# Kernel optimization log

Hardware: AMD Instinct MI355X
Metric: run time of the kernel (lower is better)

Reference implementation:

```python
import jax, jax.numpy as jnp
import numpy as np

N, E = 50000, 800000
F_IN, HID, H, LBL = 512, 16, 8, 40
HC = HID * H  # 128
BN_EPS = 1e-5
ELU_ALPHA = 0.2
NEG_SLOPE = 0.2


def setup_inputs() -> dict:
    key = jax.random.key(0)
    ks = jax.random.split(key, 32)
    inp = {}
    inp['x'] = jax.random.normal(ks[0], (N, F_IN), dtype=jnp.float32)
    inp['edge_index'] = jax.random.randint(ks[1], (2, E), 0, N, dtype=jnp.int32)
    # layer 0: F_IN -> (H, HID), concat
    inp['W0'] = jax.random.normal(ks[2], (F_IN, HC), dtype=jnp.float32) * 0.05
    inp['as0'] = jax.random.normal(ks[3], (H, HID), dtype=jnp.float32) * 0.1
    inp['ad0'] = jax.random.normal(ks[4], (H, HID), dtype=jnp.float32) * 0.1
    inp['b0'] = jnp.zeros((HC,), jnp.float32)
    inp['g0'] = jnp.ones((HC,), jnp.float32)
    inp['be0'] = jnp.zeros((HC,), jnp.float32)
    inp['rm0'] = jnp.zeros((HC,), jnp.float32)
    inp['rv0'] = jnp.ones((HC,), jnp.float32)
    # layer 1: HC -> (H, HID), concat
    inp['W1'] = jax.random.normal(ks[5], (HC, HC), dtype=jnp.float32) * 0.1
    inp['as1'] = jax.random.normal(ks[6], (H, HID), dtype=jnp.float32) * 0.1
    inp['ad1'] = jax.random.normal(ks[7], (H, HID), dtype=jnp.float32) * 0.1
    inp['b1'] = jnp.zeros((HC,), jnp.float32)
    inp['g1'] = jnp.ones((HC,), jnp.float32)
    inp['be1'] = jnp.zeros((HC,), jnp.float32)
    inp['rm1'] = jnp.zeros((HC,), jnp.float32)
    inp['rv1'] = jnp.ones((HC,), jnp.float32)
    # layer 2: HC -> (1, LBL), mean (concat=False)
    inp['W2'] = jax.random.normal(ks[8], (HC, LBL), dtype=jnp.float32) * 0.1
    inp['as2'] = jax.random.normal(ks[9], (1, LBL), dtype=jnp.float32) * 0.1
    inp['ad2'] = jax.random.normal(ks[10], (1, LBL), dtype=jnp.float32) * 0.1
    inp['b2'] = jnp.zeros((LBL,), jnp.float32)
    return inp


def _gat_conv(xf, src, dst, W, a_src, a_dst, b, heads, out_ch, concat):
    # PyG GATConv (eval): linear -> per-head attn logits -> segment softmax over dst -> scatter-add
    n = xf.shape[0]
    h = (xf @ W).reshape(n, heads, out_ch)            # [N,H,C]
    alpha_s = jnp.einsum('nhc,hc->nh', h, a_src)      # [N,H]
    alpha_d = jnp.einsum('nhc,hc->nh', h, a_dst)
    e = jax.nn.leaky_relu(alpha_s[src] + alpha_d[dst], NEG_SLOPE)  # [Etot,H]
    m = jax.ops.segment_max(e, dst, num_segments=n)
    e = jnp.exp(e - m[dst])
    s = jax.ops.segment_sum(e, dst, num_segments=n)
    alpha = e / (s[dst] + 1e-16)                      # [Etot,H]
    msg = alpha[:, :, None] * h[src]                  # [Etot,H,C]
    out = jax.ops.segment_sum(msg, dst, num_segments=n)  # [N,H,C]
    out = out.reshape(n, heads * out_ch) if concat else out.mean(axis=1)
    return out + b


def _bn_elu(xf, g, be, rm, rv):
    y = (xf - rm) * (g * jax.lax.rsqrt(rv + BN_EPS)) + be
    return jnp.where(y > 0, y, ELU_ALPHA * jnp.expm1(y))


def reference(x, edge_index, W0, as0, ad0, b0, g0, be0, rm0, rv0,
              W1, as1, ad1, b1, g1, be1, rm1, rv1, W2, as2, ad2, b2):
    n = x.shape[0]
    # add self-loops (PyG GATConv default add_self_loops=True)
    loops = jnp.arange(n, dtype=edge_index.dtype)
    src = jnp.concatenate([edge_index[0], loops])
    dst = jnp.concatenate([edge_index[1], loops])
    h = _gat_conv(x, src, dst, W0, as0, ad0, b0, H, HID, True)
    h = _bn_elu(h, g0, be0, rm0, rv0)
    h = _gat_conv(h, src, dst, W1, as1, ad1, b1, H, HID, True)
    h = _bn_elu(h, g1, be1, rm1, rv1)
    out = _gat_conv(h, src, dst, W2, as2, ad2, b2, 1, LBL, False)
    return out
```

## Files before the change

kernel.cpp:

```cpp
#include <hip/hip_runtime.h>
#include <hip/hip_bf16.h>
#include <cstdint>
#include <cstddef>

#define NN 50000
#define EE 800000
#define FIN 512
#define HIDC 16
#define NH 8
#define HCH 128
#define NLBL 40
#define NLBLP 48
#define ETOT (EE + NN)
#define NEG_SLOPE 0.2f
#define ELU_A 0.2f
#define BN_EPS 1e-5f
#define SCH 8192
#define NCHK 7

typedef __attribute__((ext_vector_type(8))) short bf16x8;
typedef __attribute__((ext_vector_type(4))) short bf16x4;
typedef __attribute__((ext_vector_type(4))) float f32x4;

__device__ inline short f2b(float f) {
    __hip_bfloat16 h = __float2bfloat16(f);
    return *reinterpret_cast<short*>(&h);
}
__device__ inline float blo(unsigned int u) {
    union { unsigned int u; float f; } v; v.u = u << 16; return v.f;
}
__device__ inline float bhi(unsigned int u) {
    union { unsigned int u; float f; } v; v.u = u & 0xffff0000u; return v.f;
}

__global__ __launch_bounds__(256) void k_prep(const float* __restrict__ W0, short* __restrict__ Wt0,
                                              const float* __restrict__ W1, short* __restrict__ Wt1,
                                              const float* __restrict__ W2, short* __restrict__ Wt2,
                                              const int* __restrict__ ei, int* __restrict__ deg)
{
    int b = blockIdx.x;
    int tid = threadIdx.x;
    if (b < 256) {
        int idx = b * 256 + tid;
        int n = idx >> 9, k = idx & 511;
        Wt0[idx] = f2b(W0[(size_t)k * HCH + n]);
        return;
    }
    b -= 256;
    if (b < 64) {
        int idx = b * 256 + tid;
        int n = idx >> 7, k = idx & 127;
        Wt1[idx] = f2b(W1[(size_t)k * HCH + n]);
        return;
    }
    b -= 64;
    if (b < 24) {
        int idx = b * 256 + tid;
        int n = idx >> 7, k = idx & 127;
        Wt2[idx] = f2b(n < NLBL ? W2[(size_t)k * NLBL + n] : 0.f);
        return;
    }
    b -= 24;
    {
        int e = b * 256 + tid;
        if (e < ETOT) {
            int dst = (e < EE) ? ei[EE + e] : (e - EE);
            atomicAdd(&deg[dst], 1);
        }
    }
}

__global__ __launch_bounds__(1024) void k_scan1(const int* __restrict__ deg,
                                                int* __restrict__ row_ptr,
                                                int* __restrict__ tot)
{
    __shared__ int sm[1024];
    int b = blockIdx.x, tid = threadIdx.x;
    int i0 = b * SCH + tid * 8;
    int v[8];
    int s = 0;
    #pragma unroll
    for (int j = 0; j < 8; ++j) {
        int i = i0 + j;
        v[j] = (i < NN) ? deg[i] : 0;
        s += v[j];
    }
    sm[tid] = s;
    __syncthreads();
    for (int ofs = 1; ofs < 1024; ofs <<= 1) {
        int t = (tid >= ofs) ? sm[tid - ofs] : 0;
        __syncthreads();
        sm[tid] += t;
        __syncthreads();
    }
    int excl = sm[tid] - s;
    #pragma unroll
    for (int j = 0; j < 8; ++j) {
        int i = i0 + j;
        if (i < NN) row_ptr[i] = excl;
        excl += v[j];
    }
    if (tid == 1023) tot[b] = sm[1023];
}

__global__ __launch_bounds__(64) void k_scan2(const int* __restrict__ tot,
                                              int* __restrict__ totp,
                                              int* __restrict__ row_ptr)
{
    if (threadIdx.x == 0) {
        int run = 0;
        for (int i = 0; i < NCHK; ++i) { totp[i] = run; run += tot[i]; }
        row_ptr[NN] = run;
    }
}

__global__ __launch_bounds__(256) void k_scan3(int* __restrict__ row_ptr,
                                               int* __restrict__ cursor,
                                               const int* __restrict__ totp)
{
    int i = blockIdx.x * 256 + threadIdx.x;
    if (i < NN) {
        int v = row_ptr[i] + totp[i / SCH];
        row_ptr[i] = v;
        cursor[i] = v;
    }
}

__global__ __launch_bounds__(256) void k_scatter(const int* __restrict__ ei,
                                                 int* __restrict__ cursor,
                                                 int* __restrict__ csr_src)
{
    int e = blockIdx.x * blockDim.x + threadIdx.x;
    if (e >= ETOT) return;
    int src, dst;
    if (e < EE) { src = ei[e]; dst = ei[EE + e]; }
    else        { src = dst = e - EE; }
    int pos = atomicAdd(&cursor[dst], 1);
    csr_src[pos] = src;
}

template<int KDIM, bool A_BF16>
__global__ __launch_bounds__(512, 4) void k_gemm2(const void* __restrict__ Ap,
                                                  const short* __restrict__ Wt,
                                                  short* __restrict__ C,
                                                  int M,
                                                  const float* __restrict__ a_s,
                                                  const float* __restrict__ a_d,
                                                  float* __restrict__ as_o,
                                                  float* __restrict__ ad_o)
{
    constexpr int KCH  = 64;
    constexpr int NCH  = KDIM / KCH;
    constexpr int LROW = KCH + 8;
    __shared__ short As[64 * LROW];
    __shared__ short Bs[128 * LROW];

    const int tid  = threadIdx.x;
    const int wv   = tid >> 6;
    const int lane = tid & 63;
    const int quad = lane >> 4;
    const int col  = lane & 15;
    const int wr   = wv >> 1;
    const int wn   = wv & 1;
    const int rowbase = blockIdx.x * 64;

    const float* Af = (const float*)Ap;
    const short* Ab = (const short*)Ap;

    float4 paA[2], paB[2];
    bf16x8 pabA, pabB;
    bf16x8 pbA[2], pbB[2];

    auto loadA = [&](int c, float4* pa, bf16x8& pab) {
        if constexpr (A_BF16) {
            int gr = rowbase + (tid >> 3);
            gr = gr < M ? gr : M - 1;
            pab = *(const bf16x8*)(Ab + (size_t)gr * KDIM + c * KCH + (tid & 7) * 8);
        } else {
            #pragma unroll
            for (int r = 0; r < 2; ++r) {
                int gr = rowbase + r * 32 + (tid >> 4);
                gr = gr < M ? gr : M - 1;
                pa[r] = *(const float4*)(Af + (size_t)gr * KDIM + c * KCH + (tid & 15) * 4);
            }
        }
    };
    auto loadB = [&](int c, bf16x8* pb) {
        #pragma unroll
        for (int r = 0; r < 2; ++r) {
            int n = r * 64 + (tid >> 3);
            pb[r] = *(const bf16x8*)(Wt + (size_t)n * KDIM + c * KCH + (tid & 7) * 8);
        }
    };
    auto writeAB = [&](const float4* pa, const bf16x8& pab, const bf16x8* pb) {
        if constexpr (A_BF16) {
            int row = tid >> 3;
            *(bf16x8*)(As + row * LROW + (tid & 7) * 8) = pab;
        } else {
            #pragma unroll
            for (int r = 0; r < 2; ++r) {
                int row = r * 32 + (tid >> 4);
                bf16x4 w;
                w[0] = f2b(pa[r].x); w[1] = f2b(pa[r].y);
                w[2] = f2b(pa[r].z); w[3] = f2b(pa[r].w);
                *(bf16x4*)(As + row * LROW + (tid & 15) * 4) = w;
            }
        }
        #pragma unroll
        for (int r = 0; r < 2; ++r) {
            int n = r * 64 + (tid >> 3);
            *(bf16x8*)(Bs + n * LROW + (tid & 7) * 8) = pb[r];
        }
    };

    f32x4 acc[4];
    #pragma unroll
    for (int t = 0; t < 4; ++t) acc[t] = (f32x4){0.f, 0.f, 0.f, 0.f};

    loadA(0, paA, pabA); loadB(0, pbA);
    if constexpr (NCH > 1) { loadA(1, paB, pabB); loadB(1, pbB); }

    #pragma unroll
    for (int c = 0; c < NCH; ++c) {
        if (c & 1) writeAB(paB, pabB, pbB);
        else       writeAB(paA, pabA, pbA);
        __syncthreads();
        if (c + 2 < NCH) {
            if (c & 1) { loadA(c + 2, paB, pabB); loadB(c + 2, pbB); }
            else       { loadA(c + 2, paA, pabA); loadB(c + 2, pbA); }
        }
        #pragma unroll
        for (int s = 0; s < KCH / 32; ++s) {
            bf16x8 af = *(const bf16x8*)(As + (wr * 16 + col) * LROW + s * 32 + quad * 8);
            #pragma unroll
            for (int t = 0; t < 4; ++t) {
                bf16x8 bf = *(const bf16x8*)(Bs + (wn * 64 + t * 16 + col) * LROW + s * 32 + quad * 8);
                acc[t] = __builtin_amdgcn_mfma_f32_16x16x32_bf16(af, bf, acc[t], 0, 0, 0);
            }
        }
        if (c + 1 < NCH) __syncthreads();
    }

    const int mb = rowbase + wr * 16 + quad * 4;

    #pragma unroll
    for (int t = 0; t < 4; ++t) {
        int cc = wn * 64 + t * 16 + col;
        #pragma unroll
        for (int r = 0; r < 4; ++r) {
            int m = mb + r;
            if (m < M) C[(size_t)m * HCH + cc] = f2b(acc[t][r]);
        }
    }

    #pragma unroll
    for (int t = 0; t < 4; ++t) {
        int hh = wn * 4 + t;
        float ws = a_s[hh * HIDC + col];
        float wd = a_d[hh * HIDC + col];
        #pragma unroll
        for (int r = 0; r < 4; ++r) {
            float vs = acc[t][r] * ws;
            float vd = acc[t][r] * wd;
            vs += __shfl_xor(vs, 1);  vd += __shfl_xor(vd, 1);
            vs += __shfl_xor(vs, 2);  vd += __shfl_xor(vd, 2);
            vs += __shfl_xor(vs, 4);  vd += __shfl_xor(vd, 4);
            vs += __shfl_xor(vs, 8);  vd += __shfl_xor(vd, 8);
            int m = mb + r;
            if (col == 0 && m < M) {
                as_o[m * NH + hh] = vs;
                ad_o[m * NH + hh] = vd;
            }
        }
    }
}

template<int KDIM, int NTILES, bool A_BF16>
__global__ __launch_bounds__(256) void k_gemm_lds(const void* __restrict__ Ap,
                                                  const short* __restrict__ Wt,
                                                  short* __restrict__ C,
                                                  int M, int N,
                                                  const float* __restrict__ a_s2,
                                                  const float* __restrict__ a_d2,
                                                  float* __restrict__ as_o,
                                                  float* __restrict__ ad_o)
{
    constexpr int NFULL = NTILES * 16;
    constexpr int KCH = 128;
    constexpr int NK = KDIM / 32;
    constexpr int NCH = KDIM / KCH;
    constexpr int LROW = KCH + 8;
    __shared__ short Bs[NFULL * LROW];

    const int tid  = threadIdx.x;
    const int wave = tid >> 6;
    const int lane = tid & 63;
    const int quad = lane >> 4;
    const int col  = lane & 15;
    const int row  = blockIdx.x * 64 + wave * 16 + col;
    const int arow = row < M ? row : M - 1;

    f32x4 acc[NTILES];
    #pragma unroll
    for (int t = 0; t < NTILES; ++t) acc[t] = (f32x4){0.f, 0.f, 0.f, 0.f};

    bf16x8 arB[4];
    float4 arF[4][2];
    const short* Ab = (const short*)Ap;
    const float* Af = (const float*)Ap;
    auto pf = [&](int ks) {
        if (ks >= NK) return;
        if (A_BF16) {
            arB[ks & 3] = *(const bf16x8*)(Ab + (size_t)arow * KDIM + ks * 32 + quad * 8);
        } else {
            const float4* p = (const float4*)(Af + (size_t)arow * KDIM + ks * 32 + quad * 8);
            arF[ks & 3][0] = p[0];
            arF[ks & 3][1] = p[1];
        }
    };
    pf(0); pf(1); pf(2); pf(3);

    for (int c = 0; c < NCH; ++c) {
        const int k0 = c * KCH;
        constexpr int TOT8 = NFULL * (KCH / 8);
        #pragma unroll
        for (int i = tid; i < TOT8; i += 256) {
            int n  = i >> 4;
            int kk = i & 15;
            bf16x8 v = *(const bf16x8*)(Wt + (size_t)n * KDIM + k0 + kk * 8);
            *(bf16x8*)(Bs + n * LROW + kk * 8) = v;
        }
        __syncthreads();
        #pragma unroll
        for (int s = 0; s < KCH / 32; ++s) {
            const int ks = c * (KCH / 32) + s;
            bf16x8 afrag;
            if (A_BF16) {
                afrag = arB[ks & 3];
            } else {
                float4 v0 = arF[ks & 3][0], v1 = arF[ks & 3][1];
                afrag[0] = f2b(v0.x); afrag[1] = f2b(v0.y);
                afrag[2] = f2b(v0.z); afrag[3] = f2b(v0.w);
                afrag[4] = f2b(v1.x); afrag[5] = f2b(v1.y);
                afrag[6] = f2b(v1.z); afrag[7] = f2b(v1.w);
            }
            pf(ks + 4);
            #pragma unroll
            for (int t = 0; t < NTILES; ++t) {
                bf16x8 bfrag = *(const bf16x8*)(Bs + (t * 16 + col) * LROW + s * 32 + quad * 8);
                acc[t] = __builtin_amdgcn_mfma_f32_16x16x32_bf16(afrag, bfrag, acc[t], 0, 0, 0);
            }
        }
        if (c + 1 < NCH) __syncthreads();
    }

    const int mbase = blockIdx.x * 64 + wave * 16 + quad * 4;
    #pragma unroll
    for (int t = 0; t < NTILES; ++t) {
        int cc = t * 16 + col;
        if (cc < N) {
            #pragma unroll
            for (int r = 0; r < 4; ++r) {
                int m = mbase + r;
                if (m < M) C[(size_t)m * N + cc] = f2b(acc[t][r]);
            }
        }
    }

    float vs[4] = {0.f, 0.f, 0.f, 0.f};
    float vd[4] = {0.f, 0.f, 0.f, 0.f};
    #pragma unroll
    for (int t = 0; t < NTILES; ++t) {
        int cc = t * 16 + col;
        float ws = cc < NLBL ? a_s2[cc] : 0.f;
        float wd = cc < NLBL ? a_d2[cc] : 0.f;
        #pragma unroll
        for (int r = 0; r < 4; ++r) {
            vs[r] += acc[t][r] * ws;
            vd[r] += acc[t][r] * wd;
        }
    }
    #pragma unroll
    for (int r = 0; r < 4; ++r) {
        float s = vs[r], d = vd[r];
        s += __shfl_xor(s, 1);  d += __shfl_xor(d, 1);
        s += __shfl_xor(s, 2);  d += __shfl_xor(d, 2);
        s += __shfl_xor(s, 4);  d += __shfl_xor(d, 4);
        s += __shfl_xor(s, 8);  d += __shfl_xor(d, 8);
        int m = mbase + r;
        if (col == 0 && m < M) {
            as_o[m] = s;
            ad_o[m] = d;
        }
    }
}

__global__ __launch_bounds__(256) void k_agg(const int* __restrict__ row_ptr,
                                             const int* __restrict__ csr_src,
                                             const unsigned short* __restrict__ h,
                                             const float* __restrict__ as,
                                             const float* __restrict__ ad,
                                             const float* __restrict__ b,
                                             const float* __restrict__ g,
                                             const float* __restrict__ be,
                                             const float* __restrict__ rm,
                                             const float* __restrict__ rv,
                                             short* __restrict__ out)
{
    int n = blockIdx.x * 4 + (threadIdx.x >> 6);
    if (n >= NN) return;
    int lane = threadIdx.x & 63;
    int half = lane >> 5;
    int c4 = lane & 31;
    int hh = c4 >> 2;
    float adv = ad[n * NH + hh];
    float a0 = 0.f, a1 = 0.f, a2 = 0.f, a3 = 0.f, sw = 0.f;
    int jb = row_ptr[n], je = row_ptr[n + 1];
    int j = jb + half;
    for (; j + 14 < je; j += 16) {
        int s[8];
        #pragma unroll
        for (int q = 0; q < 8; ++q) s[q] = csr_src[j + 2 * q];
        float l[8];
        uint2 u[8];
        #pragma unroll
        for (int q = 0; q < 8; ++q) {
            l[q] = as[s[q] * NH + hh] + adv;
            u[q] = *(const uint2*)(h + (size_t)s[q] * HCH + 4 * c4);
        }
        #pragma unroll
        for (int q = 0; q < 8; ++q) {
            float lq = l[q] > 0.f ? l[q] : NEG_SLOPE * l[q];
            float w = __expf(lq);
            sw += w;
            a0 += w * blo(u[q].x);
            a1 += w * bhi(u[q].x);
            a2 += w * blo(u[q].y);
            a3 += w * bhi(u[q].y);
        }
    }
    for (; j + 6 < je; j += 8) {
        int s0 = csr_src[j];
        int s1 = csr_src[j + 2];
        int s2 = csr_src[j + 4];
        int s3 = csr_src[j + 6];
        float l0 = as[s0 * NH + hh] + adv;
        float l1 = as[s1 * NH + hh] + adv;
        float l2 = as[s2 * NH + hh] + adv;
        float l3 = as[s3 * NH + hh] + adv;
        uint2 u0 = *(const uint2*)(h + (size_t)s0 * HCH + 4 * c4);
        uint2 u1 = *(const uint2*)(h + (size_t)s1 * HCH + 4 * c4);
        uint2 u2 = *(const uint2*)(h + (size_t)s2 * HCH + 4 * c4);
        uint2 u3 = *(const uint2*)(h + (size_t)s3 * HCH + 4 * c4);
        l0 = l0 > 0.f ? l0 : NEG_SLOPE * l0;
        l1 = l1 > 0.f ? l1 : NEG_SLOPE * l1;
        l2 = l2 > 0.f ? l2 : NEG_SLOPE * l2;
        l3 = l3 > 0.f ? l3 : NEG_SLOPE * l3;
        float w0 = __expf(l0), w1 = __expf(l1), w2 = __expf(l2), w3 = __expf(l3);
        sw += (w0 + w1) + (w2 + w3);
        a0 += w0 * blo(u0.x) + w1 * blo(u1.x) + w2 * blo(u2.x) + w3 * blo(u3.x);
        a1 += w0 * bhi(u0.x) + w1 * bhi(u1.x) + w2 * bhi(u2.x) + w3 * bhi(u3.x);
        a2 += w0 * blo(u0.y) + w1 * blo(u1.y) + w2 * blo(u2.y) + w3 * blo(u3.y);
        a3 += w0 * bhi(u0.y) + w1 * bhi(u1.y) + w2 * bhi(u2.y) + w3 * bhi(u3.y);
    }
    for (; j < je; j += 2) {
        int s0 = csr_src[j];
        float l0 = as[s0 * NH + hh] + adv;
        uint2 u0 = *(const uint2*)(h + (size_t)s0 * HCH + 4 * c4);
        l0 = l0 > 0.f ? l0 : NEG_SLOPE * l0;
        float w0 = __expf(l0);
        sw += w0;
        a0 += w0 * blo(u0.x);
        a1 += w0 * bhi(u0.x);
        a2 += w0 * blo(u0.y);
        a3 += w0 * bhi(u0.y);
    }
    a0 += __shfl_down(a0, 32);
    a1 += __shfl_down(a1, 32);
    a2 += __shfl_down(a2, 32);
    a3 += __shfl_down(a3, 32);
    sw += __shfl_down(sw, 32);
    if (half == 0) {
        int c = 4 * c4;
        float inv = 1.f / (sw + 1e-16f);
        float4 bv  = *(const float4*)(b + c);
        float4 gv  = *(const float4*)(g + c);
        float4 bev = *(const float4*)(be + c);
        float4 rmv = *(const float4*)(rm + c);
        float4 rvv = *(const float4*)(rv + c);
        float r0 = a0 * inv + bv.x;
        float r1 = a1 * inv + bv.y;
        float r2 = a2 * inv + bv.z;
        float r3 = a3 * inv + bv.w;
        r0 = (r0 - rmv.x) * (gv.x * rsqrtf(rvv.x + BN_EPS)) + bev.x;
        r1 = (r1 - rmv.y) * (gv.y * rsqrtf(rvv.y + BN_EPS)) + bev.y;
        r2 = (r2 - rmv.z) * (gv.z * rsqrtf(rvv.z + BN_EPS)) + bev.z;
        r3 = (r3 - rmv.w) * (gv.w * rsqrtf(rvv.w + BN_EPS)) + bev.w;
        r0 = r0 > 0.f ? r0 : ELU_A * expm1f(r0);
        r1 = r1 > 0.f ? r1 : ELU_A * expm1f(r1);
        r2 = r2 > 0.f ? r2 : ELU_A * expm1f(r2);
        r3 = r3 > 0.f ? r3 : ELU_A * expm1f(r3);
        unsigned int lo = (unsigned int)(unsigned short)f2b(r0) |
                          ((unsigned int)(unsigned short)f2b(r1) << 16);
        unsigned int hi = (unsigned int)(unsigned short)f2b(r2) |
                          ((unsigned int)(unsigned short)f2b(r3) << 16);
        *(uint2*)(out + (size_t)n * HCH + c) = make_uint2(lo, hi);
    }
}

__global__ __launch_bounds__(256) void k_agg2(const int* __restrict__ row_ptr,
                                              const int* __restrict__ csr_src,
                                              const unsigned short* __restrict__ h2,
                                              const float* __restrict__ as,
                                              const float* __restrict__ ad,
                                              const float* __restrict__ b,
                                              float* __restrict__ out)
{
    int n = blockIdx.x * 4 + (threadIdx.x >> 6);
    if (n >= NN) return;
    int lane = threadIdx.x & 63;
    int half = lane >> 5;
    int c2 = lane & 31;
    bool act = c2 < 20;
    int coff = act ? 2 * c2 : 0;
    float adv = ad[n];
    float acc0 = 0.f, acc1 = 0.f, sw = 0.f;
    int jb = row_ptr[n], je = row_ptr[n + 1];
    int j = jb + half;
    for (; j + 14 < je; j += 16) {
        int s[8];
        #pragma unroll
        for (int q = 0; q < 8; ++q) s[q] = csr_src[j + 2 * q];
        float l[8];
        unsigned int u[8];
        #pragma unroll
        for (int q = 0; q < 8; ++q) {
            l[q] = as[s[q]] + adv;
            u[q] = *(const unsigned int*)(h2 + (size_t)s[q] * NLBL + coff);
        }
        #pragma unroll
        for (int q = 0; q < 8; ++q) {
            float lq = l[q] > 0.f ? l[q] : NEG_SLOPE * l[q];
            float w = __expf(lq);
            sw += w;
            if (act) {
                acc0 += w * blo(u[q]);
                acc1 += w * bhi(u[q]);
            }
        }
    }
    for (; j + 6 < je; j += 8) {
        int s0 = csr_src[j];
        int s1 = csr_src[j + 2];
        int s2 = csr_src[j + 4];
        int s3 = csr_src[j + 6];
        float l0 = as[s0] + adv;
        float l1 = as[s1] + adv;
        float l2 = as[s2] + adv;
        float l3 = as[s3] + adv;
        unsigned int u0 = *(const unsigned int*)(h2 + (size_t)s0 * NLBL + coff);
        unsigned int u1 = *(const unsigned int*)(h2 + (size_t)s1 * NLBL + coff);
        unsigned int u2 = *(const unsigned int*)(h2 + (size_t)s2 * NLBL + coff);
        unsigned int u3 = *(const unsigned int*)(h2 + (size_t)s3 * NLBL + coff);
        l0 = l0 > 0.f ? l0 : NEG_SLOPE * l0;
        l1 = l1 > 0.f ? l1 : NEG_SLOPE * l1;
        l2 = l2 > 0.f ? l2 : NEG_SLOPE * l2;
        l3 = l3 > 0.f ? l3 : NEG_SLOPE * l3;
        float w0 = __expf(l0), w1 = __expf(l1), w2 = __expf(l2), w3 = __expf(l3);
        sw += (w0 + w1) + (w2 + w3);
        if (act) {
            acc0 += w0 * blo(u0) + w1 * blo(u1) + w2 * blo(u2) + w3 * blo(u3);
            acc1 += w0 * bhi(u0) + w1 * bhi(u1) + w2 * bhi(u2) + w3 * bhi(u3);
        }
    }
    for (; j < je; j += 2) {
        int s = csr_src[j];
        float l = as[s] + adv;
        unsigned int u = *(const unsigned int*)(h2 + (size_t)s * NLBL + coff);
        l = l > 0.f ? l : NEG_SLOPE * l;
        float w = __expf(l);
        sw += w;
        if (act) {
            acc0 += w * blo(u);
            acc1 += w * bhi(u);
        }
    }
    float acc0b = __shfl_down(acc0, 32);
    float acc1b = __shfl_down(acc1, 32);
    float swb   = __shfl_down(sw, 32);
    if (half == 0 && act) {
        acc0 += acc0b; acc1 += acc1b; sw += swb;
        float inv = 1.f / (sw + 1e-16f);
        out[(size_t)n * NLBL + 2 * c2]     = acc0 * inv + b[2 * c2];
        out[(size_t)n * NLBL + 2 * c2 + 1] = acc1 * inv + b[2 * c2 + 1];
    }
}

extern "C" void kernel_launch(void* const* d_in, const int* in_sizes, int n_in,
                              void* d_out, int out_size, void* d_ws, size_t ws_size,
                              hipStream_t stream)
{
    const float* x   = (const float*)d_in[0];
    const int*   ei  = (const int*)d_in[1];
    const float* W0  = (const float*)d_in[2];
    const float* as0 = (const float*)d_in[3];
    const float* ad0 = (const float*)d_in[4];
    const float* b0  = (const float*)d_in[5];
    const float* g0  = (const float*)d_in[6];
    const float* be0 = (const float*)d_in[7];
    const float* rm0 = (const float*)d_in[8];
    const float* rv0 = (const float*)d_in[9];
    const float* W1  = (const float*)d_in[10];
    const float* as1 = (const float*)d_in[11];
    const float* ad1 = (const float*)d_in[12];
    const float* b1  = (const float*)d_in[13];
    const float* g1  = (const float*)d_in[14];
    const float* be1 = (const float*)d_in[15];
    const float* rm1 = (const float*)d_in[16];
    const float* rv1 = (const float*)d_in[17];
    const float* W2  = (const float*)d_in[18];
    const float* a_s2 = (const float*)d_in[19];
    const float* a_d2 = (const float*)d_in[20];
    const float* b2  = (const float*)d_in[21];
    float* out = (float*)d_out;

    char* ws = (char*)d_ws;
    size_t off = 0;
    auto alloc = [&](size_t bytes) {
        void* p = (void*)(ws + off);
        off += (bytes + 255) & ~(size_t)255;
        return p;
    };
    short* hbuf   = (short*)alloc((size_t)NN * HCH * 2);
    short* fbuf   = (short*)alloc((size_t)NN * HCH * 2);
    float* asb    = (float*)alloc((size_t)NN * NH * 4);
    float* adb    = (float*)alloc((size_t)NN * NH * 4);
    int*   deg    = (int*)alloc((size_t)NN * 4);
    int*   rowp   = (int*)alloc((size_t)(NN + 1) * 4);
    int*   cursor = (int*)alloc((size_t)NN * 4);
    int*   csrs   = (int*)alloc((size_t)ETOT * 4);
    short* Wt0    = (short*)alloc((size_t)HCH * FIN * 2);
    short* Wt1    = (short*)alloc((size_t)HCH * HCH * 2);
    short* Wt2    = (short*)alloc((size_t)NLBLP * HCH * 2);
    int*   tot    = (int*)alloc(64 * 4);
    int*   totp   = (int*)alloc(64 * 4);
    short* h2     = hbuf;

    const int T = 256;
    const int gN4 = (NN + 3) / 4;
    const int gM  = (NN + 63) / 64;
    const int gPrep = 256 + 64 + 24 + (ETOT + T - 1) / T;
    const int gE  = (ETOT + T - 1) / T;

    hipMemsetAsync(deg, 0, (size_t)NN * 4, stream);
    k_prep<<<gPrep, T, 0, stream>>>(W0, Wt0, W1, Wt1, W2, Wt2, ei, deg);

    k_scan1<<<NCHK, 1024, 0, stream>>>(deg, rowp, tot);
    k_scan2<<<1, 64, 0, stream>>>(tot, totp, rowp);
    k_scan3<<<(NN + T - 1) / T, T, 0, stream>>>(rowp, cursor, totp);
    k_scatter<<<gE, T, 0, stream>>>(ei, cursor, csrs);

    k_gemm2<FIN, false><<<gM, 512, 0, stream>>>(x, Wt0, hbuf, NN, as0, ad0, asb, adb);
    k_agg<<<gN4, T, 0, stream>>>(rowp, csrs, (const unsigned short*)hbuf, asb, adb,
                                 b0, g0, be0, rm0, rv0, fbuf);

    k_gemm2<HCH, true><<<gM, 512, 0, stream>>>(fbuf, Wt1, hbuf, NN, as1, ad1, asb, adb);
    k_agg<<<gN4, T, 0, stream>>>(rowp, csrs, (const unsigned short*)hbuf, asb, adb,
                                 b1, g1, be1, rm1, rv1, fbuf);

    k_gemm_lds<HCH, 3, true><<<gM, T, 0, stream>>>(fbuf, Wt2, h2, NN, NLBL,
                                                   a_s2, a_d2, asb, adb);
    k_agg2<<<gN4, T, 0, stream>>>(rowp, csrs, (const unsigned short*)h2, asb, adb, b2, out);
}
```

Baseline: 460.7 us.

## Pre-convert x to chunk-major bf16 and widen GEMM K-chunk to 128

```diff
diff --git a/kernel.cpp b/kernel.cpp
--- a/kernel.cpp
+++ b/kernel.cpp
@@ -36,7 +36,8 @@
 __global__ __launch_bounds__(256) void k_prep(const float* __restrict__ W0, short* __restrict__ Wt0,
                                               const float* __restrict__ W1, short* __restrict__ Wt1,
                                               const float* __restrict__ W2, short* __restrict__ Wt2,
-                                              const int* __restrict__ ei, int* __restrict__ deg)
+                                              const int* __restrict__ ei, int* __restrict__ deg,
+                                              const float* __restrict__ x, short* __restrict__ xc)
 {
     int b = blockIdx.x;
     int tid = threadIdx.x;
@@ -61,11 +62,29 @@
         return;
     }
     b -= 24;
-    {
+    if (b < 3321) {
         int e = b * 256 + tid;
         if (e < ETOT) {
             int dst = (e < EE) ? ei[EE + e] : (e - EE);
             atomicAdd(&deg[dst], 1);
+        }
+        return;
+    }
+    b -= 3321;
+    {
+        int t = b * 256 + tid;
+        if (t < NN * (FIN / 8)) {
+            int idx = t * 8;
+            int row = idx >> 9;
+            int ko  = idx & 511;
+            int c   = ko >> 7;
+            int kk  = ko & 127;
+            const float4* p = (const float4*)(x + (size_t)row * FIN + ko);
+            float4 v0 = p[0], v1 = p[1];
+            bf16x8 w;
+            w[0] = f2b(v0.x); w[1] = f2b(v0.y); w[2] = f2b(v0.z); w[3] = f2b(v0.w);
+            w[4] = f2b(v1.x); w[5] = f2b(v1.y); w[6] = f2b(v1.z); w[7] = f2b(v1.w);
+            *(bf16x8*)(xc + ((size_t)c * NN + row) * 128 + kk) = w;
         }
     }
 }
@@ -139,8 +158,8 @@
     csr_src[pos] = src;
 }
 
-template<int KDIM, bool A_BF16>
-__global__ __launch_bounds__(512, 4) void k_gemm2(const void* __restrict__ Ap,
+template<int KDIM, bool CHUNK_MAJOR>
+__global__ __launch_bounds__(512, 4) void k_gemm2(const short* __restrict__ Ab,
                                                   const short* __restrict__ Wt,
                                                   short* __restrict__ C,
                                                   int M,
@@ -149,7 +168,7 @@
                                                   float* __restrict__ as_o,
                                                   float* __restrict__ ad_o)
 {
-    constexpr int KCH  = 64;
+    constexpr int KCH  = 128;
     constexpr int NCH  = KDIM / KCH;
     constexpr int LROW = KCH + 8;
     __shared__ short As[64 * LROW];
@@ -164,71 +183,49 @@
     const int wn   = wv & 1;
     const int rowbase = blockIdx.x * 64;
 
-    const float* Af = (const float*)Ap;
-    const short* Ab = (const short*)Ap;
-
-    float4 paA[2], paB[2];
-    bf16x8 pabA, pabB;
-    bf16x8 pbA[2], pbB[2];
-
-    auto loadA = [&](int c, float4* pa, bf16x8& pab) {
-        if constexpr (A_BF16) {
-            int gr = rowbase + (tid >> 3);
+    bf16x8 pab[2];
+    bf16x8 pb[4];
+
+    auto loadA = [&](int c) {
+        #pragma unroll
+        for (int r = 0; r < 2; ++r) {
+            int gr = rowbase + r * 32 + (tid >> 4);
             gr = gr < M ? gr : M - 1;
-            pab = *(const bf16x8*)(Ab + (size_t)gr * KDIM + c * KCH + (tid & 7) * 8);
-        } else {
-            #pragma unroll
-            for (int r = 0; r < 2; ++r) {
-                int gr = rowbase + r * 32 + (tid >> 4);
-                gr = gr < M ? gr : M - 1;
-                pa[r] = *(const float4*)(Af + (size_t)gr * KDIM + c * KCH + (tid & 15) * 4);
-            }
+            size_t base = CHUNK_MAJOR ? ((size_t)c * M + gr) * KCH
+                                      : (size_t)gr * KDIM + (size_t)c * KCH;
+            pab[r] = *(const bf16x8*)(Ab + base + (tid & 15) * 8);
         }
     };
-    auto loadB = [&](int c, bf16x8* pb) {
+    auto loadB = [&](int c) {
+        #pragma unroll
+        for (int r = 0; r < 4; ++r) {
+            int n = r * 32 + (tid >> 4);
+            pb[r] = *(const bf16x8*)(Wt + (size_t)n * KDIM + (size_t)c * KCH + (tid & 15) * 8);
+        }
+    };
+    auto writeAB = [&]() {
         #pragma unroll
         for (int r = 0; r < 2; ++r) {
-            int n = r * 64 + (tid >> 3);
-            pb[r] = *(const bf16x8*)(Wt + (size_t)n * KDIM + c * KCH + (tid & 7) * 8);
+            int row = r * 32 + (tid >> 4);
+            *(bf16x8*)(As + row * LROW + (tid & 15) * 8) = pab[r];
+        }
+        #pragma unroll
+        for (int r = 0; r < 4; ++r) {
+            int n = r * 32 + (tid >> 4);
+            *(bf16x8*)(Bs + n * LROW + (tid & 15) * 8) = pb[r];
         }
     };
-    auto writeAB = [&](const float4* pa, const bf16x8& pab, const bf16x8* pb) {
-        if constexpr (A_BF16) {
-            int row = tid >> 3;
-            *(bf16x8*)(As + row * LROW + (tid & 7) * 8) = pab;
-        } else {
-            #pragma unroll
-            for (int r = 0; r < 2; ++r) {
-                int row = r * 32 + (tid >> 4);
-                bf16x4 w;
-                w[0] = f2b(pa[r].x); w[1] = f2b(pa[r].y);
-                w[2] = f2b(pa[r].z); w[3] = f2b(pa[r].w);
-                *(bf16x4*)(As + row * LROW + (tid & 15) * 4) = w;
-            }
-        }
-        #pragma unroll
-        for (int r = 0; r < 2; ++r) {
-            int n = r * 64 + (tid >> 3);
-            *(bf16x8*)(Bs + n * LROW + (tid & 7) * 8) = pb[r];
-        }
-    };
 
     f32x4 acc[4];
     #pragma unroll
     for (int t = 0; t < 4; ++t) acc[t] = (f32x4){0.f, 0.f, 0.f, 0.f};
 
-    loadA(0, paA, pabA); loadB(0, pbA);
-    if constexpr (NCH > 1) { loadA(1, paB, pabB); loadB(1, pbB); }
-
-    #pragma unroll
+    loadA(0); loadB(0);
+
     for (int c = 0; c < NCH; ++c) {
-        if (c & 1) writeAB(paB, pabB, pbB);
-        else       writeAB(paA, pabA, pbA);
+        writeAB();
         __syncthreads();
-        if (c + 2 < NCH) {
-            if (c & 1) { loadA(c + 2, paB, pabB); loadB(c + 2, pbB); }
-            else       { loadA(c + 2, paA, pabA); loadB(c + 2, pbA); }
-        }
+        if (c + 1 < NCH) { loadA(c + 1); loadB(c + 1); }
         #pragma unroll
         for (int s = 0; s < KCH / 32; ++s) {
             bf16x8 af = *(const bf16x8*)(As + (wr * 16 + col) * LROW + s * 32 + quad * 8);
@@ -275,8 +272,8 @@
     }
 }
 
-template<int KDIM, int NTILES, bool A_BF16>
-__global__ __launch_bounds__(256) void k_gemm_lds(const void* __restrict__ Ap,
+template<int KDIM, int NTILES>
+__global__ __launch_bounds__(256) void k_gemm_lds(const short* __restrict__ Ab,
                                                   const short* __restrict__ Wt,
                                                   short* __restrict__ C,
                                                   int M, int N,
@@ -305,18 +302,9 @@
     for (int t = 0; t < NTILES; ++t) acc[t] = (f32x4){0.f, 0.f, 0.f, 0.f};
 
     bf16x8 arB[4];
-    float4 arF[4][2];
-    const short* Ab = (const short*)Ap;
-    const float* Af = (const float*)Ap;
     auto pf = [&](int ks) {
         if (ks >= NK) return;
-        if (A_BF16) {
-            arB[ks & 3] = *(const bf16x8*)(Ab + (size_t)arow * KDIM + ks * 32 + quad * 8);
-        } else {
-            const float4* p = (const float4*)(Af + (size_t)arow * KDIM + ks * 32 + quad * 8);
-            arF[ks & 3][0] = p[0];
-            arF[ks & 3][1] = p[1];
-        }
+        arB[ks & 3] = *(const bf16x8*)(Ab + (size_t)arow * KDIM + ks * 32 + quad * 8);
     };
     pf(0); pf(1); pf(2); pf(3);
 
@@ -334,16 +322,7 @@
         #pragma unroll
         for (int s = 0; s < KCH / 32; ++s) {
             const int ks = c * (KCH / 32) + s;
-            bf16x8 afrag;
-            if (A_BF16) {
-                afrag = arB[ks & 3];
-            } else {
-                float4 v0 = arF[ks & 3][0], v1 = arF[ks & 3][1];
-                afrag[0] = f2b(v0.x); afrag[1] = f2b(v0.y);
-                afrag[2] = f2b(v0.z); afrag[3] = f2b(v0.w);
-                afrag[4] = f2b(v1.x); afrag[5] = f2b(v1.y);
-                afrag[6] = f2b(v1.z); afrag[7] = f2b(v1.w);
-            }
+            bf16x8 afrag = arB[ks & 3];
             pf(ks + 4);
             #pragma unroll
             for (int t = 0; t < NTILES; ++t) {
@@ -633,6 +612,7 @@
     };
     short* hbuf   = (short*)alloc((size_t)NN * HCH * 2);
     short* fbuf   = (short*)alloc((size_t)NN * HCH * 2);
+    short* xc     = (short*)alloc((size_t)4 * NN * 128 * 2);
     float* asb    = (float*)alloc((size_t)NN * NH * 4);
     float* adb    = (float*)alloc((size_t)NN * NH * 4);
     int*   deg    = (int*)alloc((size_t)NN * 4);
@@ -649,26 +629,28 @@
     const int T = 256;
     const int gN4 = (NN + 3) / 4;
     const int gM  = (NN + 63) / 64;
-    const int gPrep = 256 + 64 + 24 + (ETOT + T - 1) / T;
-    const int gE  = (ETOT + T - 1) / T;
+    const int gHist = (ETOT + T - 1) / T;
+    const int gConv = (NN * (FIN / 8) + T - 1) / T;
+    const int gPrep = 256 + 64 + 24 + gHist + gConv;
+    const int gE  = gHist;
 
     hipMemsetAsync(deg, 0, (size_t)NN * 4, stream);
-    k_prep<<<gPrep, T, 0, stream>>>(W0, Wt0, W1, Wt1, W2, Wt2, ei, deg);
+    k_prep<<<gPrep, T, 0, stream>>>(W0, Wt0, W1, Wt1, W2, Wt2, ei, deg, x, xc);
 
     k_scan1<<<NCHK, 1024, 0, stream>>>(deg, rowp, tot);
     k_scan2<<<1, 64, 0, stream>>>(tot, totp, rowp);
     k_scan3<<<(NN + T - 1) / T, T, 0, stream>>>(rowp, cursor, totp);
     k_scatter<<<gE, T, 0, stream>>>(ei, cursor, csrs);
 
-    k_gemm2<FIN, false><<<gM, 512, 0, stream>>>(x, Wt0, hbuf, NN, as0, ad0, asb, adb);
+    k_gemm2<FIN, true><<<gM, 512, 0, stream>>>(xc, Wt0, hbuf, NN, as0, ad0, asb, adb);
     k_agg<<<gN4, T, 0, stream>>>(rowp, csrs, (const unsigned short*)hbuf, asb, adb,
                                  b0, g0, be0, rm0, rv0, fbuf);
 
-    k_gemm2<HCH, true><<<gM, 512, 0, stream>>>(fbuf, Wt1, hbuf, NN, as1, ad1, asb, adb);
+    k_gemm2<HCH, false><<<gM, 512, 0, stream>>>(fbuf, Wt1, hbuf, NN, as1, ad1, asb, adb);
     k_agg<<<gN4, T, 0, stream>>>(rowp, csrs, (const unsigned short*)hbuf, asb, adb,
                                  b1, g1, be1, rm1, rv1, fbuf);
 
-    k_gemm_lds<HCH, 3, true><<<gM, T, 0, stream>>>(fbuf, Wt2, h2, NN, NLBL,
-                                                   a_s2, a_d2, asb, adb);
+    k_gemm_lds<HCH, 3><<<gM, T, 0, stream>>>(fbuf, Wt2, h2, NN, NLBL,
+                                             a_s2, a_d2, asb, adb);
     k_agg2<<<gN4, T, 0, stream>>>(rowp, csrs, (const unsigned short*)h2, asb, adb, b2, out);
 }
```

Measured after the change: 460.5 us. About the same (-0.0%).
